# Optimization experiments

Measured on AMD Instinct MI355X. Metric: run time of the kernel, lower is better.

## Reference

```python
import jax, jax.numpy as jnp
import numpy as np

E = 8          # num_experts
TOP_K = 2      # router top-k
ALPHA = 1.702  # swigluoai alpha
LIMIT = 7.0    # swigluoai clamp limit


def setup_inputs() -> dict:
    key = jax.random.key(0)
    ks = jax.random.split(key, 7)
    B, S, H, I = 2, 1024, 1024, 1024
    s = 1.0 / np.sqrt(H)  # keep activations O(1), realistic init scale
    return {
        "x": jax.random.normal(ks[0], (B, S, H), jnp.float32),
        "router_weight": jax.random.normal(ks[1], (E, H), jnp.float32) * s,
        "router_bias": jax.random.normal(ks[2], (E,), jnp.float32) * 0.01,
        "w1": jax.random.normal(ks[3], (E, H, 2 * I), jnp.float32) * s,  # interleaved gate/up
        "w1_bias": jax.random.normal(ks[4], (E, 2 * I), jnp.float32) * 0.01,
        "w2": jax.random.normal(ks[5], (E, I, H), jnp.float32) * s,
        "w2_bias": jax.random.normal(ks[6], (E, H), jnp.float32) * 0.01,
    }


def _moe(x, router_weight, router_bias, w1, w1_bias, w2, w2_bias):
    B, S, H = x.shape
    xf = x.reshape(-1, H)                                   # [T, H]
    # ---- router: softmax over expert logits, then top-k ----
    logits = xf @ router_weight.T + router_bias             # [T, E]
    probs = jax.nn.softmax(logits, axis=-1)
    expert_weights, expert_ids = jax.lax.top_k(probs, TOP_K)  # [T, k]
    # combine weights scattered to dense [T, E] (no normalization: normalize_expert_weights=None)
    combine = jnp.sum(jax.nn.one_hot(expert_ids, E, dtype=xf.dtype)
                      * expert_weights[..., None], axis=1)  # [T, E]
    # ---- grouped MLP, expressed densely per expert (reference semantics) ----
    h = jnp.einsum('th,ehi->eti', xf, w1) + w1_bias[:, None, :]   # [E, T, 2I]
    gate = h[..., 0::2]                                          # interleaved layout
    up = h[..., 1::2]
    gate = jnp.minimum(gate, LIMIT)                              # swigluoai: clamp gate max
    up = jnp.clip(up, -LIMIT, LIMIT)                             # clamp up both sides
    glu = gate * jax.nn.sigmoid(gate * ALPHA)
    act = (up + 1.0) * glu                                       # [E, T, I]
    y = jnp.einsum('eti,eih->eth', act, w2) + w2_bias[:, None, :]  # [E, T, H]
    out = jnp.einsum('eth,te->th', y, combine)                   # weighted combine
    return out.reshape(B, S, H), expert_weights


def reference(x, router_weight, router_bias, w1, w1_bias, w2, w2_bias):
    return _moe(x, router_weight, router_bias, w1, w1_bias, w2, w2_bias)
```

## Files before the change

kernel.cpp:

```cpp
#include <hip/hip_runtime.h>
#include <cstdint>
#include <cstddef>

typedef unsigned short u16;
typedef short bf16x8 __attribute__((ext_vector_type(8)));
typedef float floatx4 __attribute__((ext_vector_type(4)));

#define GLD16(gp, sp) __builtin_amdgcn_global_load_lds(                      \
    (const __attribute__((address_space(1))) void*)(gp),                     \
    (__attribute__((address_space(3))) void*)(sp), 16, 0, 0)

#define VWAIT(N) asm volatile("s_waitcnt vmcnt(" #N ")" ::: "memory")
#define BARF()                                                               \
  do {                                                                       \
    __builtin_amdgcn_sched_barrier(0);                                       \
    __builtin_amdgcn_s_barrier();                                            \
    __builtin_amdgcn_sched_barrier(0);                                       \
  } while (0)

__device__ __forceinline__ u16 f2bf(float f) {
  unsigned u = __float_as_uint(f);
  u += 0x7fffu + ((u >> 16) & 1u);
  return (u16)(u >> 16);
}

__global__ void transpose_cvt2_kernel(const float* __restrict__ w1, u16* __restrict__ w1t,
                                      const float* __restrict__ w2, u16* __restrict__ w2t) {
  __shared__ float tile[32][33];
  int z = blockIdx.z;
  const float* in; u16* out; int C;
  if (z < 8) { in = w1; out = w1t; C = 2048; }
  else { if (blockIdx.x >= 32) return; in = w2; out = w2t; C = 1024; z -= 8; }
  const int R = 1024;
  size_t base = (size_t)z * (size_t)R * (size_t)C;
  int c0 = blockIdx.x * 32, r0 = blockIdx.y * 32;
  int tx = threadIdx.x, ty = threadIdx.y;
#pragma unroll
  for (int k = 0; k < 32; k += 8)
    tile[ty + k][tx] = in[base + (size_t)(r0 + ty + k) * C + (c0 + tx)];
  __syncthreads();
#pragma unroll
  for (int k = 0; k < 32; k += 8)
    out[base + (size_t)(c0 + ty + k) * R + (r0 + tx)] = f2bf(tile[tx][ty + k]);
}

__global__ void router_kernel(const float* __restrict__ x, const float* __restrict__ rw,
                              const float* __restrict__ rb, float* __restrict__ ew,
                              int* __restrict__ eids, float* __restrict__ eprobs) {
  const int wave = threadIdx.x >> 6, lane = threadIdx.x & 63;
  const int t = blockIdx.x * 4 + wave;
  const float4* xv = (const float4*)(x + (size_t)t * 1024);
  float acc[8];
#pragma unroll
  for (int e = 0; e < 8; ++e) acc[e] = 0.f;
  for (int j = lane; j < 256; j += 64) {
    float4 xx = xv[j];
#pragma unroll
    for (int e = 0; e < 8; ++e) {
      float4 wv = ((const float4*)(rw + (size_t)e * 1024))[j];
      acc[e] += xx.x * wv.x + xx.y * wv.y + xx.z * wv.z + xx.w * wv.w;
    }
  }
#pragma unroll
  for (int e = 0; e < 8; ++e) {
    float v = acc[e];
#pragma unroll
    for (int off = 32; off > 0; off >>= 1) v += __shfl_down(v, off);
    acc[e] = v;
  }
  if (lane == 0) {
    float p[8];
    float mx = -1e30f;
#pragma unroll
    for (int e = 0; e < 8; ++e) { p[e] = acc[e] + rb[e]; mx = fmaxf(mx, p[e]); }
    float sum = 0.f;
#pragma unroll
    for (int e = 0; e < 8; ++e) { p[e] = __expf(p[e] - mx); sum += p[e]; }
    float inv = 1.f / sum;
#pragma unroll
    for (int e = 0; e < 8; ++e) p[e] *= inv;
    int i0 = 0;
#pragma unroll
    for (int e = 1; e < 8; ++e) if (p[e] > p[i0]) i0 = e;
    int i1 = (i0 == 0) ? 1 : 0;
#pragma unroll
    for (int e = 0; e < 8; ++e) if (e != i0 && e != i1 && p[e] > p[i1]) i1 = e;
    ew[t * 2 + 0] = p[i0];
    ew[t * 2 + 1] = p[i1];
    eids[t * 2 + 0] = i0;
    eids[t * 2 + 1] = i1;
    eprobs[t * 2 + 0] = p[i0];
    eprobs[t * 2 + 1] = p[i1];
  }
}

__global__ void build_lists_kernel(const int* __restrict__ eids, const float* __restrict__ eprobs,
                                   int* __restrict__ row_token, float* __restrict__ row_scale,
                                   int* __restrict__ tok2slot, int* __restrict__ meta) {
  __shared__ int cnt[8], base[8], cur[8];
  const int tid = threadIdx.x;
  if (tid < 8) { cnt[tid] = 0; cur[tid] = 0; }
  __syncthreads();
  for (int t = tid; t < 2048; t += 256) {
    atomicAdd(&cnt[eids[t * 2 + 0]], 1);
    atomicAdd(&cnt[eids[t * 2 + 1]], 1);
  }
  __syncthreads();
  if (tid == 0) {
    int off = 0, w = 0;
    for (int e = 0; e < 8; ++e) {
      base[e] = off;
      meta[48 + e] = off;
      int nb = (cnt[e] + 127) >> 7;
      for (int rb = 0; rb < nb; ++rb) meta[1 + w++] = (e << 8) | rb;
      off += nb << 7;
    }
    meta[0] = w;
  }
  __syncthreads();
  for (int s = tid; s < 5120; s += 256) { row_token[s] = -1; row_scale[s] = 0.f; }
  __syncthreads();
  for (int t = tid; t < 2048; t += 256) {
#pragma unroll
    for (int k = 0; k < 2; ++k) {
      int e = eids[t * 2 + k];
      int s = base[e] + atomicAdd(&cur[e], 1);
      row_token[s] = t;
      row_scale[s] = eprobs[t * 2 + k];
      tok2slot[t * 2 + k] = s;
    }
  }
}

__global__ void gather_x_kernel(const float* __restrict__ x, const int* __restrict__ row_token,
                                u16* __restrict__ xg) {
  const int s = blockIdx.x;
  int tk = row_token[s];
  if (tk < 0) tk = 0;
  const float4* src = (const float4*)(x + (size_t)tk * 1024);
  ushort4* dst = (ushort4*)(xg + (size_t)s * 1024);
  const int t = threadIdx.x;
  float4 v = src[t];
  ushort4 o;
  o.x = f2bf(v.x); o.y = f2bf(v.y); o.z = f2bf(v.z); o.w = f2bf(v.w);
  dst[t] = o;
}

__device__ __forceinline__ void g1_compute(const u16* AsR, const u16* BsR, int wr, int wc,
                                           int lane, floatx4 (&acc)[4][4]) {
  bf16x8 af[4], bfr[4];
#pragma unroll
  for (int mi = 0; mi < 4; ++mi) af[mi] = *(const bf16x8*)(AsR + (wr * 4 + mi) * 512 + lane * 8);
#pragma unroll
  for (int ni = 0; ni < 4; ++ni) bfr[ni] = *(const bf16x8*)(BsR + (wc * 4 + ni) * 512 + lane * 8);
  __builtin_amdgcn_s_setprio(1);
#pragma unroll
  for (int mi = 0; mi < 4; ++mi)
#pragma unroll
    for (int ni = 0; ni < 4; ++ni)
      acc[mi][ni] = __builtin_amdgcn_mfma_f32_16x16x32_bf16(af[mi], bfr[ni], acc[mi][ni], 0, 0, 0);
  __builtin_amdgcn_s_setprio(0);
}

__global__ __launch_bounds__(256) void gemm1_act_kernel(
    const u16* __restrict__ xg, const u16* __restrict__ w1t,
    const float* __restrict__ w1b, const float* __restrict__ row_scale,
    const int* __restrict__ meta, u16* __restrict__ actS) {
  if ((int)blockIdx.x >= meta[0]) return;
  __shared__ __align__(16) u16 As[3][128 * 32];
  __shared__ __align__(16) u16 Bs[3][128 * 32];
  const int w = meta[1 + blockIdx.x];
  const int e = w >> 8, rb = w & 255;
  const int slotB = meta[48 + e] + rb * 128;
  const int colBase = blockIdx.y * 128;
  const int tid = threadIdx.x, lane = tid & 63, wave = tid >> 6;
  const int row16 = lane & 15, chunk = lane >> 4;
  const u16* Bt = w1t + (size_t)e * 2048 * 1024;
  const u16* aP[2]; const u16* bP[2];
#pragma unroll
  for (int r = 0; r < 2; ++r) {
    int g = r * 4 + wave;
    aP[r] = xg + (size_t)(slotB + g * 16 + row16) * 1024 + chunk * 8;
    bP[r] = Bt + (size_t)(colBase + g * 16 + row16) * 1024 + chunk * 8;
  }
  const int wr = wave >> 1, wc = wave & 1;
  floatx4 acc[4][4];
#pragma unroll
  for (int mi = 0; mi < 4; ++mi)
#pragma unroll
    for (int ni = 0; ni < 4; ++ni) acc[mi][ni] = floatx4{0.f, 0.f, 0.f, 0.f};

#define G1_STAGE(W, KT)                                                      \
  {                                                                          \
    const int kk = (KT) * 32;                                                \
    GLD16(aP[0] + kk, As[W] + wave * 512);                                   \
    GLD16(bP[0] + kk, Bs[W] + wave * 512);                                   \
    GLD16(aP[1] + kk, As[W] + (4 + wave) * 512);                             \
    GLD16(bP[1] + kk, Bs[W] + (4 + wave) * 512);                             \
  }

  G1_STAGE(0, 0);
  G1_STAGE(1, 1);

#pragma unroll 1
  for (int kt = 0; kt < 30; kt += 3) {
    G1_STAGE(2, kt + 2); VWAIT(8); BARF();
    g1_compute(As[0], Bs[0], wr, wc, lane, acc); BARF();
    G1_STAGE(0, kt + 3); VWAIT(8); BARF();
    g1_compute(As[1], Bs[1], wr, wc, lane, acc); BARF();
    G1_STAGE(1, kt + 4); VWAIT(8); BARF();
    g1_compute(As[2], Bs[2], wr, wc, lane, acc); BARF();
  }
  VWAIT(4); BARF();
  g1_compute(As[0], Bs[0], wr, wc, lane, acc); BARF();
  VWAIT(0); BARF();
  g1_compute(As[1], Bs[1], wr, wc, lane, acc);
#undef G1_STAGE

  const int cl = lane & 15, ql = lane >> 4;
#pragma unroll
  for (int mi = 0; mi < 4; ++mi) {
#pragma unroll
    for (int r = 0; r < 4; ++r) {
      const int slot = slotB + wr * 64 + mi * 16 + ql * 4 + r;
      const float c = row_scale[slot];
#pragma unroll
      for (int ni = 0; ni < 4; ++ni) {
        const int n = colBase + wc * 64 + ni * 16 + cl;
        float v = acc[mi][ni][r] + w1b[e * 2048 + n];
        float o = __shfl_xor(v, 1);
        if ((lane & 1) == 0) {
          float g = fminf(v, 7.f);
          float u = fminf(fmaxf(o, -7.f), 7.f);
          float sg = 1.f / (1.f + __expf(-1.702f * g));
          float a = (u + 1.f) * (g * sg);
          actS[(size_t)slot * 1024 + (n >> 1)] = f2bf(c * a);
        }
      }
    }
  }
}

__device__ __forceinline__ void g2_compute(const u16* AsR, const u16* BsR, int wr, int wc,
                                           int lane, floatx4 (&acc)[4][2]) {
  bf16x8 af[4], bfr[2];
#pragma unroll
  for (int mi = 0; mi < 4; ++mi) af[mi] = *(const bf16x8*)(AsR + (wr * 4 + mi) * 512 + lane * 8);
#pragma unroll
  for (int ni = 0; ni < 2; ++ni) bfr[ni] = *(const bf16x8*)(BsR + (wc * 2 + ni) * 512 + lane * 8);
  __builtin_amdgcn_s_setprio(1);
#pragma unroll
  for (int mi = 0; mi < 4; ++mi)
#pragma unroll
    for (int ni = 0; ni < 2; ++ni)
      acc[mi][ni] = __builtin_amdgcn_mfma_f32_16x16x32_bf16(af[mi], bfr[ni], acc[mi][ni], 0, 0, 0);
  __builtin_amdgcn_s_setprio(0);
}

__global__ __launch_bounds__(256) void gemm2_kernel(
    const u16* __restrict__ actS, const u16* __restrict__ w2t,
    const int* __restrict__ meta, float* __restrict__ y) {
  if ((int)blockIdx.x >= meta[0]) return;
  __shared__ __align__(16) u16 As[3][128 * 32];
  __shared__ __align__(16) u16 Bs[3][64 * 32];
  const int w = meta[1 + blockIdx.x];
  const int e = w >> 8, rb = w & 255;
  const int slotB = meta[48 + e] + rb * 128;
  const int colBase = blockIdx.y * 64;
  const int tid = threadIdx.x, lane = tid & 63, wave = tid >> 6;
  const int row16 = lane & 15, chunk = lane >> 4;
  const u16* Bt = w2t + (size_t)e * 1024 * 1024;
  const u16* aP[2]; const u16* bP1;
#pragma unroll
  for (int r = 0; r < 2; ++r) {
    int g = r * 4 + wave;
    aP[r] = actS + (size_t)(slotB + g * 16 + row16) * 1024 + chunk * 8;
  }
  bP1 = Bt + (size_t)(colBase + wave * 16 + row16) * 1024 + chunk * 8;
  const int wr = wave >> 1, wc = wave & 1;
  floatx4 acc[4][2];
#pragma unroll
  for (int mi = 0; mi < 4; ++mi)
#pragma unroll
    for (int ni = 0; ni < 2; ++ni) acc[mi][ni] = floatx4{0.f, 0.f, 0.f, 0.f};

#define G2_STAGE(W, KT)                                                      \
  {                                                                          \
    const int kk = (KT) * 32;                                                \
    GLD16(aP[0] + kk, As[W] + wave * 512);                                   \
    GLD16(aP[1] + kk, As[W] + (4 + wave) * 512);                             \
    GLD16(bP1 + kk, Bs[W] + wave * 512);                                     \
  }

  G2_STAGE(0, 0);
  G2_STAGE(1, 1);

#pragma unroll 1
  for (int kt = 0; kt < 30; kt += 3) {
    G2_STAGE(2, kt + 2); VWAIT(6); BARF();
    g2_compute(As[0], Bs[0], wr, wc, lane, acc); BARF();
    G2_STAGE(0, kt + 3); VWAIT(6); BARF();
    g2_compute(As[1], Bs[1], wr, wc, lane, acc); BARF();
    G2_STAGE(1, kt + 4); VWAIT(6); BARF();
    g2_compute(As[2], Bs[2], wr, wc, lane, acc); BARF();
  }
  VWAIT(3); BARF();
  g2_compute(As[0], Bs[0], wr, wc, lane, acc); BARF();
  VWAIT(0); BARF();
  g2_compute(As[1], Bs[1], wr, wc, lane, acc);
#undef G2_STAGE

  const int cl = lane & 15, ql = lane >> 4;
#pragma unroll
  for (int mi = 0; mi < 4; ++mi)
#pragma unroll
    for (int r = 0; r < 4; ++r) {
      const int slot = slotB + wr * 64 + mi * 16 + ql * 4 + r;
#pragma unroll
      for (int ni = 0; ni < 2; ++ni) {
        const int col = colBase + wc * 32 + ni * 16 + cl;
        y[(size_t)slot * 1024 + col] = acc[mi][ni][r];
      }
    }
}

__global__ void combine_kernel(const float* __restrict__ y, const int* __restrict__ eids,
                               const float* __restrict__ eprobs, const int* __restrict__ tok2slot,
                               const float* __restrict__ w2b, float* __restrict__ out) {
  int idx = blockIdx.x * 256 + threadIdx.x;
  int t = idx >> 10, h = idx & 1023;
  int e0 = eids[t * 2], e1 = eids[t * 2 + 1];
  int s0 = tok2slot[t * 2], s1 = tok2slot[t * 2 + 1];
  out[idx] = eprobs[t * 2] * w2b[e0 * 1024 + h] + eprobs[t * 2 + 1] * w2b[e1 * 1024 + h]
           + y[(size_t)s0 * 1024 + h] + y[(size_t)s1 * 1024 + h];
}

extern "C" void kernel_launch(void* const* d_in, const int* in_sizes, int n_in,
                              void* d_out, int out_size, void* d_ws, size_t ws_size,
                              hipStream_t stream) {
  const float* x   = (const float*)d_in[0];
  const float* rw  = (const float*)d_in[1];
  const float* rb  = (const float*)d_in[2];
  const float* w1  = (const float*)d_in[3];
  const float* w1b = (const float*)d_in[4];
  const float* w2  = (const float*)d_in[5];
  const float* w2b = (const float*)d_in[6];
  float* out = (float*)d_out;
  float* ew  = out + (size_t)2048 * 1024;

  char* ws = (char*)d_ws;
  u16* xg        = (u16*)(ws);
  u16* w1t       = (u16*)(ws + (10ull << 20));
  float* y       = (float*)(ws + (10ull << 20));
  u16* w2t       = (u16*)(ws + (42ull << 20));
  u16* actS      = (u16*)(ws + (58ull << 20));
  int* eids      = (int*)(ws + (68ull << 20));
  float* eprobs  = (float*)(ws + (68ull << 20) + (16 << 10));
  int* row_token = (int*)(ws + (68ull << 20) + (32 << 10));
  float* row_scale = (float*)(ws + (68ull << 20) + (52 << 10));
  int* meta      = (int*)(ws + (68ull << 20) + (72 << 10));
  int* tok2slot  = (int*)(ws + (68ull << 20) + (74 << 10));

  transpose_cvt2_kernel<<<dim3(64, 32, 16), dim3(32, 8), 0, stream>>>(w1, w1t, w2, w2t);
  router_kernel<<<512, 256, 0, stream>>>(x, rw, rb, ew, eids, eprobs);
  build_lists_kernel<<<1, 256, 0, stream>>>(eids, eprobs, row_token, row_scale, tok2slot, meta);
  gather_x_kernel<<<5120, 256, 0, stream>>>(x, row_token, xg);
  gemm1_act_kernel<<<dim3(40, 16), 256, 0, stream>>>(xg, w1t, w1b, row_scale, meta, actS);
  gemm2_kernel<<<dim3(40, 16), 256, 0, stream>>>(actS, w2t, meta, y);
  combine_kernel<<<8192, 256, 0, stream>>>(y, eids, eprobs, tok2slot, w2b, out);
}
```

Measured before the change: 266.7 us.

## Fuse router with wider weight transpose and deepen gemm2 K tile

Router and weight transpose/convert now run as one launch. Blocks 512 and up do the transpose with 64x64 tiles, float4 loads and ushort4 stores, while the first 512 blocks compute the router. gemm2's K-step per stage doubles from 32 to 64, halving loop iterations and barriers, at the cost of twice the LDS per stage. This removes a launch and should raise transpose bandwidth, but gemm2 occupancy may drop from the larger shared buffers.

Result: no change. 267.9 us (+0.5%).

```diff
diff --git a/kernel.cpp b/kernel.cpp
--- a/kernel.cpp
+++ b/kernel.cpp
@@ -24,31 +24,58 @@
   return (u16)(u >> 16);
 }
 
-__global__ void transpose_cvt2_kernel(const float* __restrict__ w1, u16* __restrict__ w1t,
-                                      const float* __restrict__ w2, u16* __restrict__ w2t) {
-  __shared__ float tile[32][33];
-  int z = blockIdx.z;
-  const float* in; u16* out; int C;
-  if (z < 8) { in = w1; out = w1t; C = 2048; }
-  else { if (blockIdx.x >= 32) return; in = w2; out = w2t; C = 1024; z -= 8; }
-  const int R = 1024;
-  size_t base = (size_t)z * (size_t)R * (size_t)C;
-  int c0 = blockIdx.x * 32, r0 = blockIdx.y * 32;
-  int tx = threadIdx.x, ty = threadIdx.y;
-#pragma unroll
-  for (int k = 0; k < 32; k += 8)
-    tile[ty + k][tx] = in[base + (size_t)(r0 + ty + k) * C + (c0 + tx)];
+__device__ __forceinline__ void transpose64(const float* __restrict__ inb, u16* __restrict__ outb,
+                                            int C, int r0, int c0) {
+  __shared__ float tileT[64][65];
+  const int t = threadIdx.x;
+  const int k = t & 15, w = t >> 4;
+#pragma unroll
+  for (int it = 0; it < 4; ++it) {
+    const int r = r0 + w + it * 16;
+    const float4 v = *(const float4*)(inb + (size_t)r * C + (c0 + k * 4));
+    tileT[k * 4 + 0][w + it * 16] = v.x;
+    tileT[k * 4 + 1][w + it * 16] = v.y;
+    tileT[k * 4 + 2][w + it * 16] = v.z;
+    tileT[k * 4 + 3][w + it * 16] = v.w;
+  }
   __syncthreads();
 #pragma unroll
-  for (int k = 0; k < 32; k += 8)
-    out[base + (size_t)(c0 + ty + k) * R + (r0 + tx)] = f2bf(tile[tx][ty + k]);
-}
-
-__global__ void router_kernel(const float* __restrict__ x, const float* __restrict__ rw,
-                              const float* __restrict__ rb, float* __restrict__ ew,
-                              int* __restrict__ eids, float* __restrict__ eprobs) {
+  for (int it = 0; it < 4; ++it) {
+    const int cc = w + it * 16;
+    const int r4 = k * 4;
+    ushort4 o;
+    o.x = f2bf(tileT[cc][r4 + 0]);
+    o.y = f2bf(tileT[cc][r4 + 1]);
+    o.z = f2bf(tileT[cc][r4 + 2]);
+    o.w = f2bf(tileT[cc][r4 + 3]);
+    *(ushort4*)(outb + (size_t)(c0 + cc) * 1024 + r0 + r4) = o;
+  }
+}
+
+__global__ __launch_bounds__(256) void front_kernel(
+    const float* __restrict__ x, const float* __restrict__ rw, const float* __restrict__ rb,
+    float* __restrict__ ew, int* __restrict__ eids, float* __restrict__ eprobs,
+    const float* __restrict__ w1, u16* __restrict__ w1t,
+    const float* __restrict__ w2, u16* __restrict__ w2t) {
+  const int bid = blockIdx.x;
+  if (bid >= 512) {
+    int idx = bid - 512;
+    if (idx < 4096) {
+      const int e = idx >> 9, rem = idx & 511;
+      const int ct = rem & 31, rt = rem >> 5;
+      transpose64(w1 + (size_t)e * 1024 * 2048, w1t + (size_t)e * 2048 * 1024,
+                  2048, rt * 64, ct * 64);
+    } else {
+      idx -= 4096;
+      const int e = idx >> 8, rem = idx & 255;
+      const int ct = rem & 15, rt = rem >> 4;
+      transpose64(w2 + (size_t)e * 1024 * 1024, w2t + (size_t)e * 1024 * 1024,
+                  1024, rt * 64, ct * 64);
+    }
+    return;
+  }
   const int wave = threadIdx.x >> 6, lane = threadIdx.x & 63;
-  const int t = blockIdx.x * 4 + wave;
+  const int t = bid * 4 + wave;
   const float4* xv = (const float4*)(x + (size_t)t * 1024);
   float acc[8];
 #pragma unroll
@@ -243,17 +270,25 @@
 
 __device__ __forceinline__ void g2_compute(const u16* AsR, const u16* BsR, int wr, int wc,
                                            int lane, floatx4 (&acc)[4][2]) {
-  bf16x8 af[4], bfr[2];
-#pragma unroll
-  for (int mi = 0; mi < 4; ++mi) af[mi] = *(const bf16x8*)(AsR + (wr * 4 + mi) * 512 + lane * 8);
-#pragma unroll
-  for (int ni = 0; ni < 2; ++ni) bfr[ni] = *(const bf16x8*)(BsR + (wc * 2 + ni) * 512 + lane * 8);
+  bf16x8 af[2][4], bfr[2][2];
+#pragma unroll
+  for (int kk = 0; kk < 2; ++kk)
+#pragma unroll
+    for (int mi = 0; mi < 4; ++mi)
+      af[kk][mi] = *(const bf16x8*)(AsR + (((wr * 4 + mi) * 2) + kk) * 512 + lane * 8);
+#pragma unroll
+  for (int kk = 0; kk < 2; ++kk)
+#pragma unroll
+    for (int ni = 0; ni < 2; ++ni)
+      bfr[kk][ni] = *(const bf16x8*)(BsR + (((wc * 2 + ni) * 2) + kk) * 512 + lane * 8);
   __builtin_amdgcn_s_setprio(1);
 #pragma unroll
-  for (int mi = 0; mi < 4; ++mi)
-#pragma unroll
-    for (int ni = 0; ni < 2; ++ni)
-      acc[mi][ni] = __builtin_amdgcn_mfma_f32_16x16x32_bf16(af[mi], bfr[ni], acc[mi][ni], 0, 0, 0);
+  for (int kk = 0; kk < 2; ++kk)
+#pragma unroll
+    for (int mi = 0; mi < 4; ++mi)
+#pragma unroll
+      for (int ni = 0; ni < 2; ++ni)
+        acc[mi][ni] = __builtin_amdgcn_mfma_f32_16x16x32_bf16(af[kk][mi], bfr[kk][ni], acc[mi][ni], 0, 0, 0);
   __builtin_amdgcn_s_setprio(0);
 }
 
@@ -261,8 +296,8 @@
     const u16* __restrict__ actS, const u16* __restrict__ w2t,
     const int* __restrict__ meta, float* __restrict__ y) {
   if ((int)blockIdx.x >= meta[0]) return;
-  __shared__ __align__(16) u16 As[3][128 * 32];
-  __shared__ __align__(16) u16 Bs[3][64 * 32];
+  __shared__ __align__(16) u16 As[3][128 * 64];
+  __shared__ __align__(16) u16 Bs[3][64 * 64];
   const int w = meta[1 + blockIdx.x];
   const int e = w >> 8, rb = w & 255;
   const int slotB = meta[48 + e] + rb * 128;
@@ -270,13 +305,13 @@
   const int tid = threadIdx.x, lane = tid & 63, wave = tid >> 6;
   const int row16 = lane & 15, chunk = lane >> 4;
   const u16* Bt = w2t + (size_t)e * 1024 * 1024;
-  const u16* aP[2]; const u16* bP1;
+  const u16* aP[2]; const u16* bP;
 #pragma unroll
   for (int r = 0; r < 2; ++r) {
     int g = r * 4 + wave;
     aP[r] = actS + (size_t)(slotB + g * 16 + row16) * 1024 + chunk * 8;
   }
-  bP1 = Bt + (size_t)(colBase + wave * 16 + row16) * 1024 + chunk * 8;
+  bP = Bt + (size_t)(colBase + wave * 16 + row16) * 1024 + chunk * 8;
   const int wr = wave >> 1, wc = wave & 1;
   floatx4 acc[4][2];
 #pragma unroll
@@ -286,28 +321,35 @@
 
 #define G2_STAGE(W, KT)                                                      \
   {                                                                          \
-    const int kk = (KT) * 32;                                                \
-    GLD16(aP[0] + kk, As[W] + wave * 512);                                   \
-    GLD16(aP[1] + kk, As[W] + (4 + wave) * 512);                             \
-    GLD16(bP1 + kk, Bs[W] + wave * 512);                                     \
+    const int kb = (KT) * 64;                                                \
+    GLD16(aP[0] + kb,      As[W] + (wave * 2 + 0) * 512);                    \
+    GLD16(aP[0] + kb + 32, As[W] + (wave * 2 + 1) * 512);                    \
+    GLD16(aP[1] + kb,      As[W] + ((4 + wave) * 2 + 0) * 512);              \
+    GLD16(aP[1] + kb + 32, As[W] + ((4 + wave) * 2 + 1) * 512);              \
+    GLD16(bP + kb,         Bs[W] + (wave * 2 + 0) * 512);                    \
+    GLD16(bP + kb + 32,    Bs[W] + (wave * 2 + 1) * 512);                    \
   }
 
   G2_STAGE(0, 0);
   G2_STAGE(1, 1);
 
 #pragma unroll 1
-  for (int kt = 0; kt < 30; kt += 3) {
-    G2_STAGE(2, kt + 2); VWAIT(6); BARF();
+  for (int kt = 0; kt < 12; kt += 3) {
+    G2_STAGE(2, kt + 2); VWAIT(12); BARF();
     g2_compute(As[0], Bs[0], wr, wc, lane, acc); BARF();
-    G2_STAGE(0, kt + 3); VWAIT(6); BARF();
+    G2_STAGE(0, kt + 3); VWAIT(12); BARF();
     g2_compute(As[1], Bs[1], wr, wc, lane, acc); BARF();
-    G2_STAGE(1, kt + 4); VWAIT(6); BARF();
+    G2_STAGE(1, kt + 4); VWAIT(12); BARF();
     g2_compute(As[2], Bs[2], wr, wc, lane, acc); BARF();
   }
-  VWAIT(3); BARF();
+  G2_STAGE(2, 14); VWAIT(12); BARF();
   g2_compute(As[0], Bs[0], wr, wc, lane, acc); BARF();
+  G2_STAGE(0, 15); VWAIT(12); BARF();
+  g2_compute(As[1], Bs[1], wr, wc, lane, acc); BARF();
+  VWAIT(6); BARF();
+  g2_compute(As[2], Bs[2], wr, wc, lane, acc); BARF();
   VWAIT(0); BARF();
-  g2_compute(As[1], Bs[1], wr, wc, lane, acc);
+  g2_compute(As[0], Bs[0], wr, wc, lane, acc);
 #undef G2_STAGE
 
   const int cl = lane & 15, ql = lane >> 4;
@@ -361,8 +403,8 @@
   int* meta      = (int*)(ws + (68ull << 20) + (72 << 10));
   int* tok2slot  = (int*)(ws + (68ull << 20) + (74 << 10));
 
-  transpose_cvt2_kernel<<<dim3(64, 32, 16), dim3(32, 8), 0, stream>>>(w1, w1t, w2, w2t);
-  router_kernel<<<512, 256, 0, stream>>>(x, rw, rb, ew, eids, eprobs);
+  front_kernel<<<512 + 4096 + 2048, 256, 0, stream>>>(x, rw, rb, ew, eids, eprobs,
+                                                      w1, w1t, w2, w2t);
   build_lists_kernel<<<1, 256, 0, stream>>>(eids, eprobs, row_token, row_scale, tok2slot, meta);
   gather_x_kernel<<<5120, 256, 0, stream>>>(x, row_token, xg);
   gemm1_act_kernel<<<dim3(40, 16), 256, 0, stream>>>(xg, w1t, w1b, row_scale, meta, actS);
```
